# Performance work log

Measured on AMD Instinct MI355X. Metric: run time of the kernel, lower is better.

The kernel has to match this reference:

```python
import jax, jax.numpy as jnp
import numpy as np

B, S, D, H, DFF = 2, 2048, 1024, 16, 4096
DK = D // H
EPS = 1e-6
MASK_FILL = -1.0  # original code uses -1**9 == -1 (precedence bug), NOT -1e9


def layernorm(x, gamma, beta):
    # original: (x - mean) / (std + eps), std unbiased (torch default ddof=1), scalar gamma/beta
    mean = jnp.mean(x, axis=-1, keepdims=True)
    std = jnp.std(x, axis=-1, keepdims=True, ddof=1)
    return gamma * (x - mean) / (std + EPS) + beta


def setup_inputs() -> dict:
    key = jax.random.key(0)
    ks = jax.random.split(key, 12)
    sc = 0.02
    return {
        "x": jax.random.normal(ks[0], (B, S, D), jnp.float32),
        "src_mask": jnp.ones((B, 1, 1, S), jnp.int32),
        "wq": jax.random.normal(ks[1], (D, D), jnp.float32) * sc,
        "bq": jnp.zeros((D,), jnp.float32),
        "wk": jax.random.normal(ks[2], (D, D), jnp.float32) * sc,
        "bk": jnp.zeros((D,), jnp.float32),
        "wv": jax.random.normal(ks[3], (D, D), jnp.float32) * sc,
        "bv": jnp.zeros((D,), jnp.float32),
        "wo": jax.random.normal(ks[4], (D, D), jnp.float32) * sc,
        "bo": jnp.zeros((D,), jnp.float32),
        "w1": jax.random.normal(ks[5], (D, DFF), jnp.float32) * sc,
        "b1": jnp.zeros((DFF,), jnp.float32),
        "w2": jax.random.normal(ks[6], (DFF, D), jnp.float32) * sc,
        "b2": jnp.zeros((D,), jnp.float32),
        "g1": jnp.ones((), jnp.float32),
        "be1": jnp.zeros((), jnp.float32),
        "g2": jnp.ones((), jnp.float32),
        "be2": jnp.zeros((), jnp.float32),
    }


def reference(x, src_mask, wq, bq, wk, bk, wv, bv, wo, bo,
              w1, b1, w2, b2, g1, be1, g2, be2):
    # --- residual 1: pre-LN self-attention ---
    xn = layernorm(x, g1, be1)
    q = (xn @ wq + bq).reshape(B, S, H, DK).transpose(0, 2, 1, 3)  # [B,H,S,DK]
    k = (xn @ wk + bk).reshape(B, S, H, DK).transpose(0, 2, 1, 3)
    v = (xn @ wv + bv).reshape(B, S, H, DK).transpose(0, 2, 1, 3)
    scores = jnp.einsum('bhqd,bhkd->bhqk', q, k) / jnp.sqrt(jnp.float32(DK))
    scores = jnp.where(src_mask == 0, MASK_FILL, scores)
    attn = jax.nn.softmax(scores, axis=-1)
    ctx = jnp.einsum('bhqk,bhkd->bhqd', attn, v)
    ctx = ctx.transpose(0, 2, 1, 3).reshape(B, S, D)
    attn_out = ctx @ wo + bo
    x = x + attn_out  # dropout is identity in eval

    # --- residual 2: pre-LN feed-forward ---
    xn = layernorm(x, g2, be2)
    h = jax.nn.relu(xn @ w1 + b1)
    ff_out = h @ w2 + b2
    return x + ff_out
```

## Files before the change

### kernel.cpp

```cpp
#include <hip/hip_runtime.h>

typedef unsigned short u16;
typedef __bf16 bf16x8 __attribute__((ext_vector_type(8)));
typedef float f32x4 __attribute__((ext_vector_type(4)));
typedef float f32x16 __attribute__((ext_vector_type(16)));

#define AS1U(p) ((__attribute__((address_space(1))) unsigned int*)(p))
#define AS3U(p) ((__attribute__((address_space(3))) unsigned int*)(p))

__device__ __forceinline__ u16 f2bf(float f) {
  union { float f; unsigned int i; } c; c.f = f;
  return (u16)((c.i + 0x7FFFu + ((c.i >> 16) & 1u)) >> 16);
}
__device__ __forceinline__ u16 f2bf_trunc(float f) {
  union { float f; unsigned int i; } c; c.f = f;
  return (u16)(c.i >> 16);
}
__device__ __forceinline__ unsigned cvt_pk_bf16(float lo, float hi) {
  unsigned r;
  asm("v_cvt_pk_bf16_f32 %0, %1, %2" : "=v"(r) : "v"(lo), "v"(hi));
  return r;
}
__device__ __forceinline__ void plswap(unsigned& a, unsigned& b) {
  asm("v_permlane32_swap_b32 %0, %1" : "+v"(a), "+v"(b));
}

template <int BM, int BN, int BK, int OMODE>
__global__ __launch_bounds__(256) void gemm_bt(
    const u16* __restrict__ A, long lda,
    const u16* __restrict__ B, long ldb,
    void* __restrict__ Cv, long ldc,
    int K, float scale, const float* __restrict__ bias,
    const float* __restrict__ res, long ldres, int relu) {
  constexpr int WN = (BN == 128) ? 64 : 32;
  constexpr int MI = 4, NJ = WN / 16;
  constexpr int KK = BK / 32;
  __shared__ u16 As0[BM * BK], As1[BM * BK];
  __shared__ u16 Bs0[BN * BK], Bs1[BN * BK];
  const int t = threadIdx.x;
  const int w = t >> 6, l = t & 63;
  const int wr = w >> 1, wc = w & 1;
  const int quad = l >> 4, mlo = l & 15;
  const long row0 = (long)blockIdx.x * BM;
  const long col0 = (long)blockIdx.y * BN;

  f32x4 acc[MI][NJ] = {};

  auto stage = [&](u16 (&Ad)[BM * BK], u16 (&Bd)[BN * BK], int k0) {
    if (BK == 32) {
#pragma unroll
      for (int i = 0; i < BM / 64; i++) {
        int s = t + i * 256, r = s >> 2, c = s & 3;
        const u16* g = A + (row0 + r) * lda + k0 + c * 8;
        __builtin_amdgcn_global_load_lds(AS1U(g), AS3U(&Ad[s * 8]), 16, 0, 0);
      }
#pragma unroll
      for (int i = 0; i < BN / 64; i++) {
        int s = t + i * 256, r = s >> 2, c = s & 3;
        const u16* g = B + (col0 + r) * ldb + k0 + c * 8;
        __builtin_amdgcn_global_load_lds(AS1U(g), AS3U(&Bd[s * 8]), 16, 0, 0);
      }
    } else {
#pragma unroll
      for (int i = 0; i < BM / 32; i++) {
        int s = t + i * 256, r = s >> 3, c = s & 7;
        const u16* g = A + (row0 + r) * lda + k0 + (c ^ (r & 7)) * 8;
        __builtin_amdgcn_global_load_lds(AS1U(g), AS3U(&Ad[s * 8]), 16, 0, 0);
      }
#pragma unroll
      for (int i = 0; i < BN / 32; i++) {
        int s = t + i * 256, r = s >> 3, c = s & 7;
        const u16* g = B + (col0 + r) * ldb + k0 + (c ^ (r & 7)) * 8;
        __builtin_amdgcn_global_load_lds(AS1U(g), AS3U(&Bd[s * 8]), 16, 0, 0);
      }
    }
  };
  auto compute = [&](const u16 (&Asr)[BM * BK], const u16 (&Bsr)[BN * BK]) {
#pragma unroll
    for (int kk = 0; kk < KK; kk++) {
      bf16x8 a[MI], b[NJ];
#pragma unroll
      for (int i = 0; i < MI; i++) {
        int r = wr * 64 + i * 16 + mlo;
        a[i] = (BK == 32) ? *(const bf16x8*)&Asr[(r * 4 + quad) * 8]
                          : *(const bf16x8*)&Asr[(r * 8 + ((kk * 4 + quad) ^ (r & 7))) * 8];
      }
#pragma unroll
      for (int j = 0; j < NJ; j++) {
        int r = wc * WN + j * 16 + mlo;
        b[j] = (BK == 32) ? *(const bf16x8*)&Bsr[(r * 4 + quad) * 8]
                          : *(const bf16x8*)&Bsr[(r * 8 + ((kk * 4 + quad) ^ (r & 7))) * 8];
      }
#pragma unroll
      for (int i = 0; i < MI; i++)
#pragma unroll
        for (int j = 0; j < NJ; j++)
          acc[i][j] = __builtin_amdgcn_mfma_f32_16x16x32_bf16(a[i], b[j], acc[i][j], 0, 0, 0);
    }
  };

  stage(As0, Bs0, 0);
  for (int k0 = 0; k0 < K; k0 += 2 * BK) {
    __syncthreads();
    stage(As1, Bs1, k0 + BK);
    compute(As0, Bs0);
    __syncthreads();
    if (k0 + 2 * BK < K) stage(As0, Bs0, k0 + 2 * BK);
    compute(As1, Bs1);
  }

#pragma unroll
  for (int i = 0; i < MI; i++) {
#pragma unroll
    for (int j = 0; j < NJ; j++) {
      const long gn = col0 + wc * WN + j * 16 + mlo;
      const float bv = bias ? bias[gn] : 0.0f;
#pragma unroll
      for (int r = 0; r < 4; r++) {
        const long gm = row0 + wr * 64 + i * 16 + quad * 4 + r;
        float v = acc[i][j][r] * scale + bv;
        if (relu && v < 0.0f) v = 0.0f;
        if (res) v += res[gm * ldres + gn];
        if (OMODE == 0) ((float*)Cv)[gm * ldc + gn] = v;
        else ((u16*)Cv)[gm * ldc + gn] = f2bf(v);
      }
    }
  }
}

__global__ __launch_bounds__(256, 2) void flash_attn(
    const u16* __restrict__ QKV, const u16* __restrict__ VT,
    const int* __restrict__ mask, u16* __restrict__ ctx) {
  __shared__ u16 Ks[2][64 * 64];
  __shared__ u16 Vs[2][64 * 64];
  const int t = threadIdx.x;
  const int w = t >> 6, l = t & 63;
  const int hi = l >> 5, lq = l & 31, rx = lq & 7;
  const int z = blockIdx.z, b = z >> 4, h = z & 15;
  const long q0 = (long)blockIdx.x * 128;
  const u16* Qg = QKV + (long)b * (2048L * 3072) + h * 64;
  const u16* Kg = Qg + 1024;
  const u16* Vg = VT + (long)b * (1024L * 2048) + (long)(h * 64) * 2048;
  const int* mrow = mask + b * 2048;

#pragma unroll
  for (int i = 0; i < 2; i++) {
    int s = t + i * 256, r = s >> 3, c = s & 7;
    __builtin_amdgcn_global_load_lds(AS1U(Kg + (long)r * 3072 + (c ^ (r & 7)) * 8),
                                     AS3U(&Ks[0][s * 8]), 16, 0, 0);
    __builtin_amdgcn_global_load_lds(AS1U(Vg + (long)r * 2048 + (c ^ (r & 7)) * 8),
                                     AS3U(&Vs[0][s * 8]), 16, 0, 0);
  }

  const float CS = 0.125f * 1.44269504f;
  const float CM = -1.44269504f;

  bf16x8 aq[4];
#pragma unroll
  for (int kk = 0; kk < 4; kk++) {
    const u16* g = Qg + (q0 + w * 32 + lq) * 3072 + kk * 16 + hi * 8;
    union { uint4 u; bf16x8 v; u16 s[8]; } cc; cc.u = *(const uint4*)g;
#pragma unroll
    for (int e = 0; e < 8; e++) {
      union { unsigned u; float f; } qf; qf.u = (unsigned)cc.s[e] << 16;
      cc.s[e] = f2bf(qf.f * CS);
    }
    aq[kk] = cc.v;
  }

  unsigned am = 0;
  for (int it = 0; it < 32; ++it) {
    unsigned long long bmv = __ballot(mrow[it * 64 + l] != 0);
    am |= ((bmv == ~0ull) ? 1u : 0u) << it;
  }

  f32x16 o[2] = {}, den = {};
  union { u16 s[8]; bf16x8 v; } ones;
#pragma unroll
  for (int e = 0; e < 8; e++) ones.s[e] = 0x3F80;

  for (int it = 0; it < 32; ++it) {
    const int cur = it & 1;
    __syncthreads();
    if (it + 1 < 32) {
      const int nb = 1 - cur;
      const u16* Kg2 = Kg + (long)(it + 1) * 64 * 3072;
      const u16* Vg2 = Vg + (it + 1) * 64;
#pragma unroll
      for (int i2 = 0; i2 < 2; i2++) {
        int s = t + i2 * 256, r = s >> 3, c = s & 7;
        __builtin_amdgcn_global_load_lds(AS1U(Kg2 + (long)r * 3072 + (c ^ (r & 7)) * 8),
                                         AS3U(&Ks[nb][s * 8]), 16, 0, 0);
        __builtin_amdgcn_global_load_lds(AS1U(Vg2 + (long)r * 2048 + (c ^ (r & 7)) * 8),
                                         AS3U(&Vs[nb][s * 8]), 16, 0, 0);
      }
    }
    const bool allone = (am >> it) & 1u;
    unsigned long long bm = ~0ull;
    if (!allone) bm = __ballot(mrow[it * 64 + l] != 0);

    f32x16 sa[2];
    __builtin_amdgcn_s_setprio(1);
#pragma unroll
    for (int kt = 0; kt < 2; kt++) {
      f32x16 s0 = {};
      const int rk = kt * 32 + lq;
#pragma unroll
      for (int kk = 0; kk < 4; kk++) {
        bf16x8 ak = *(const bf16x8*)&Ks[cur][(rk * 8 + ((2 * kk + hi) ^ rx)) * 8];
        s0 = __builtin_amdgcn_mfma_f32_32x32x16_bf16(ak, aq[kk], s0, 0, 0, 0);
      }
      sa[kt] = s0;
    }
    __builtin_amdgcn_s_setprio(0);

#pragma unroll
    for (int kt = 0; kt < 2; kt++) {
      float p[16];
      if (allone) {
#pragma unroll
        for (int g = 0; g < 16; g++) p[g] = __builtin_amdgcn_exp2f(sa[kt][g]);
      } else {
#pragma unroll
        for (int g = 0; g < 16; g++) {
          const int k = kt * 32 + (g & 3) + 8 * (g >> 2) + 4 * hi;
          const float s = ((bm >> k) & 1) ? sa[kt][g] : CM;
          p[g] = __builtin_amdgcn_exp2f(s);
        }
      }
      unsigned wd[4][2];
#pragma unroll
      for (int g = 0; g < 4; g++) {
        wd[g][0] = cvt_pk_bf16(p[4 * g + 0], p[4 * g + 1]);
        wd[g][1] = cvt_pk_bf16(p[4 * g + 2], p[4 * g + 3]);
      }
#pragma unroll
      for (int c = 0; c < 2; c++) {
        plswap(wd[2 * c][0], wd[2 * c + 1][0]);
        plswap(wd[2 * c][1], wd[2 * c + 1][1]);
        union { unsigned u[4]; bf16x8 v; } pa;
        pa.u[0] = wd[2 * c][0];
        pa.u[1] = wd[2 * c][1];
        pa.u[2] = wd[2 * c + 1][0];
        pa.u[3] = wd[2 * c + 1][1];
        const int cg = kt * 2 + c;
        __builtin_amdgcn_s_setprio(1);
#pragma unroll
        for (int dt = 0; dt < 2; dt++) {
          const int rv = dt * 32 + lq;
          bf16x8 bv = *(const bf16x8*)&Vs[cur][(rv * 8 + ((2 * cg + hi) ^ rx)) * 8];
          o[dt] = __builtin_amdgcn_mfma_f32_32x32x16_bf16(pa.v, bv, o[dt], 0, 0, 0);
        }
        den = __builtin_amdgcn_mfma_f32_32x32x16_bf16(pa.v, ones.v, den, 0, 0, 0);
        __builtin_amdgcn_s_setprio(0);
      }
    }
  }

  u16* cb = ctx + (long)b * (2048L * 1024) + (q0 + w * 32) * 1024 + h * 64;
#pragma unroll
  for (int g = 0; g < 16; g++) {
    const int row = (g & 3) + 8 * (g >> 2) + 4 * hi;
    const float inv = 1.0f / den[g];
    cb[(long)row * 1024 + lq] = f2bf(o[0][g] * inv);
    cb[(long)row * 1024 + 32 + lq] = f2bf(o[1][g] * inv);
  }
}

__device__ __forceinline__ void ln_row(const float* __restrict__ x, u16* __restrict__ y,
                                       const float* __restrict__ g, const float* __restrict__ b,
                                       long row, float* ss, float* s2) {
  const float* xr = x + row * 1024;
  float v[4];
  float s = 0.f, sq = 0.f;
#pragma unroll
  for (int i = 0; i < 4; i++) {
    float f = xr[threadIdx.x + i * 256];
    v[i] = f; s += f; sq += f * f;
  }
#pragma unroll
  for (int o = 32; o > 0; o >>= 1) { s += __shfl_xor(s, o, 64); sq += __shfl_xor(sq, o, 64); }
  const int w = threadIdx.x >> 6;
  if ((threadIdx.x & 63) == 0) { ss[w] = s; s2[w] = sq; }
  __syncthreads();
  s = ss[0] + ss[1] + ss[2] + ss[3];
  sq = s2[0] + s2[1] + s2[2] + s2[3];
  const float mean = s * (1.0f / 1024.0f);
  float var = (sq - s * mean) * (1.0f / 1023.0f);
  var = fmaxf(var, 0.0f);
  const float sc = g[0] / (sqrtf(var) + 1e-6f);
  const float be = b[0];
#pragma unroll
  for (int i = 0; i < 4; i++)
    y[row * 1024 + threadIdx.x + i * 256] = f2bf((v[i] - mean) * sc + be);
}

__global__ __launch_bounds__(256) void ln_kernel(const float* __restrict__ x, u16* __restrict__ y,
                                                 const float* __restrict__ g, const float* __restrict__ b) {
  __shared__ float ss[4], s2[4];
  ln_row(x, y, g, b, blockIdx.x, ss, s2);
}

__global__ __launch_bounds__(256) void prep_kernel(
    const float* __restrict__ x, const float* __restrict__ g1, const float* __restrict__ be1,
    const float* __restrict__ wq, const float* __restrict__ wk, const float* __restrict__ wv,
    const float* __restrict__ wo, const float* __restrict__ w1, const float* __restrict__ w2,
    const float* __restrict__ bq, const float* __restrict__ bk, const float* __restrict__ bv,
    u16* __restrict__ xnH, u16* __restrict__ WqkvT, u16* __restrict__ woT,
    u16* __restrict__ w1T, u16* __restrict__ w2T, float* __restrict__ biasQKV) {
  __shared__ float tile[32][33];
  __shared__ float ss[4], s2[4];
  const int bid = blockIdx.x;
  if (bid >= 12300) {
    ln_row(x, xnH, g1, be1, bid - 12300, ss, s2);
    return;
  }
  if (bid >= 12288) {
    const int i = (bid - 12288) * 256 + threadIdx.x;
    if (i < 3072) biasQKV[i] = (i < 1024) ? bq[i] : ((i < 2048) ? bk[i - 1024] : bv[i - 2048]);
    return;
  }
  const float* in; u16* out; long ldin, ldo; int ti, tiles_x;
  if (bid < 1024)      { in = wq; out = WqkvT;                     ldin = 1024; ldo = 1024; ti = bid;        tiles_x = 32; }
  else if (bid < 2048) { in = wk; out = WqkvT + (size_t)1024*1024; ldin = 1024; ldo = 1024; ti = bid - 1024; tiles_x = 32; }
  else if (bid < 3072) { in = wv; out = WqkvT + (size_t)2048*1024; ldin = 1024; ldo = 1024; ti = bid - 2048; tiles_x = 32; }
  else if (bid < 4096) { in = wo; out = woT;                       ldin = 1024; ldo = 1024; ti = bid - 3072; tiles_x = 32; }
  else if (bid < 8192) { in = w1; out = w1T;                       ldin = 4096; ldo = 1024; ti = bid - 4096; tiles_x = 128; }
  else                 { in = w2; out = w2T;                       ldin = 1024; ldo = 4096; ti = bid - 8192; tiles_x = 32; }
  const int bx = (ti % tiles_x) * 32, by = (ti / tiles_x) * 32;
  const int tx = threadIdx.x & 31, ty = threadIdx.x >> 5;
#pragma unroll
  for (int i = 0; i < 32; i += 8) tile[ty + i][tx] = in[(long)(by + ty + i) * ldin + bx + tx];
  __syncthreads();
#pragma unroll
  for (int i = 0; i < 32; i += 8)
    out[(long)(bx + ty + i) * ldo + by + tx] = f2bf(tile[tx][ty + i]);
}

__global__ __launch_bounds__(256) void ttrans1(const u16* __restrict__ in, long ldin, long siz,
                                               u16* __restrict__ out, long ldo, long soz) {
  __shared__ u16 tile[32][33];
  const long zi = (long)blockIdx.z * siz, zo = (long)blockIdx.z * soz;
  const int bx = blockIdx.x * 32, by = blockIdx.y * 32;
  const int tx = threadIdx.x & 31, ty = threadIdx.x >> 5;
#pragma unroll
  for (int i = 0; i < 32; i += 8)
    tile[ty + i][tx] = in[zi + (long)(by + ty + i) * ldin + bx + tx];
  __syncthreads();
#pragma unroll
  for (int i = 0; i < 32; i += 8)
    out[zo + (long)(bx + ty + i) * ldo + by + tx] = tile[tx][ty + i];
}

extern "C" void kernel_launch(void* const* d_in, const int* in_sizes, int n_in,
                              void* d_out, int out_size, void* d_ws, size_t ws_size,
                              hipStream_t stream) {
  const float* x   = (const float*)d_in[0];
  const int*   msk = (const int*)d_in[1];
  const float* wq  = (const float*)d_in[2];
  const float* bq  = (const float*)d_in[3];
  const float* wk  = (const float*)d_in[4];
  const float* bk  = (const float*)d_in[5];
  const float* wv  = (const float*)d_in[6];
  const float* bv  = (const float*)d_in[7];
  const float* wo  = (const float*)d_in[8];
  const float* bo  = (const float*)d_in[9];
  const float* w1  = (const float*)d_in[10];
  const float* b1  = (const float*)d_in[11];
  const float* w2  = (const float*)d_in[12];
  const float* b2  = (const float*)d_in[13];
  const float* g1  = (const float*)d_in[14];
  const float* be1 = (const float*)d_in[15];
  const float* g2  = (const float*)d_in[16];
  const float* be2 = (const float*)d_in[17];
  float* out = (float*)d_out;

  char* basep = (char*)d_ws;
  size_t off = 0;
  auto au = [&](size_t nelem) -> u16* {
    u16* r = (u16*)(basep + off);
    off += ((nelem * 2) + 255) & ~(size_t)255;
    return r;
  };
  auto afp = [&](size_t nelem) -> float* {
    float* r = (float*)(basep + off);
    off += ((nelem * 4) + 255) & ~(size_t)255;
    return r;
  };

  u16* xnH  = au((size_t)4096 * 1024);
  u16* QKV  = au((size_t)4096 * 3072);
  u16* VTH  = au((size_t)2 * 1024 * 2048);
  u16* ctxH = au((size_t)4096 * 1024);
  float* x1 = afp((size_t)4096 * 1024);
  u16* hb   = au((size_t)4096 * 4096);
  u16* WqkvT = au((size_t)3072 * 1024);
  u16* woT  = au((size_t)1024 * 1024);
  u16* w1T  = au((size_t)4096 * 1024);
  u16* w2T  = au((size_t)1024 * 4096);
  float* biasQKV = afp(3072);

  const dim3 blk(256);

  prep_kernel<<<16396, blk, 0, stream>>>(x, g1, be1, wq, wk, wv, wo, w1, w2,
                                         bq, bk, bv, xnH, WqkvT, woT, w1T, w2T, biasQKV);

  gemm_bt<128, 128, 32, 2><<<dim3(32, 24), blk, 0, stream>>>(
      xnH, 1024, WqkvT, 1024, QKV, 3072, 1024, 1.0f,
      biasQKV, (const float*)0, 0, 0);

  ttrans1<<<dim3(32, 64, 2), blk, 0, stream>>>(
      QKV + 2048, 3072, (long)2048 * 3072, VTH, 2048, (long)1024 * 2048);

  flash_attn<<<dim3(16, 1, 32), blk, 0, stream>>>(QKV, VTH, msk, ctxH);

  gemm_bt<128, 64, 64, 0><<<dim3(32, 16), blk, 0, stream>>>(
      ctxH, 1024, woT, 1024, x1, 1024, 1024, 1.0f, bo, x, 1024, 0);

  ln_kernel<<<4096, blk, 0, stream>>>(x1, xnH, g2, be2);

  gemm_bt<128, 128, 32, 2><<<dim3(32, 32), blk, 0, stream>>>(
      xnH, 1024, w1T, 1024, hb, 4096, 1024, 1.0f,
      b1, (const float*)0, 0, 1);

  gemm_bt<128, 64, 64, 0><<<dim3(32, 16), blk, 0, stream>>>(
      hb, 4096, w2T, 4096, out, 1024, 4096, 1.0f, b2, x1, 1024, 0);
}
```

Measured before the change: 356.7 us.

## Add 256x128 triple-buffered direct-to-LDS MFMA GEMM for QKV and FF1

Introduces a new 512-thread GEMM kernel with 256x128 tiles and BK=64. It uses three LDS buffers filled by global_load_lds with an XOR swizzle, 32x32x16 bf16 MFMAs, and setprio around the math. It replaces the 128x128 GEMM for the QKV projection and the first FFN matmul, aiming for more data reuse per block and better overlap of loads with compute. The large LDS footprint limits residency to one block per CU, and the QKV grid leaves a partial wave.

```diff
diff --git a/kernel.cpp b/kernel.cpp
--- a/kernel.cpp
+++ b/kernel.cpp
@@ -23,6 +23,102 @@
 }
 __device__ __forceinline__ void plswap(unsigned& a, unsigned& b) {
   asm("v_permlane32_swap_b32 %0, %1" : "+v"(a), "+v"(b));
+}
+
+template <int OMODE>
+__global__ __launch_bounds__(512, 2) void gemm3(
+    const u16* __restrict__ A, long lda,
+    const u16* __restrict__ B, long ldb,
+    void* __restrict__ Cv, long ldc,
+    int K, const float* __restrict__ bias,
+    const float* __restrict__ res, long ldres, int relu) {
+  __shared__ u16 As[3][256 * 64];
+  __shared__ u16 Bs[3][128 * 64];
+  const int t = threadIdx.x;
+  const int w = t >> 6, l = t & 63;
+  const int hi = l >> 5, lq = l & 31;
+  const int wm = w >> 1, wn = w & 1;
+  const long row0 = (long)blockIdx.x * 256;
+  const long col0 = (long)blockIdx.y * 128;
+
+  auto stage = [&](int slot, int k0) {
+#pragma unroll
+    for (int i = 0; i < 4; i++) {
+      int s = t + i * 512, r = s >> 3, c = s & 7;
+      __builtin_amdgcn_global_load_lds(AS1U(A + (row0 + r) * lda + k0 + (c ^ (r & 7)) * 8),
+                                       AS3U(&As[slot][s * 8]), 16, 0, 0);
+    }
+#pragma unroll
+    for (int i = 0; i < 2; i++) {
+      int s = t + i * 512, r = s >> 3, c = s & 7;
+      __builtin_amdgcn_global_load_lds(AS1U(B + (col0 + r) * ldb + k0 + (c ^ (r & 7)) * 8),
+                                       AS3U(&Bs[slot][s * 8]), 16, 0, 0);
+    }
+  };
+
+  f32x16 acc[2][2] = {};
+  const int NT = K >> 6;
+
+  stage(0, 0);
+  stage(1, 64);
+  asm volatile("s_waitcnt vmcnt(6)" ::: "memory");
+  __builtin_amdgcn_s_barrier();
+  __builtin_amdgcn_sched_barrier(0);
+
+  int s0 = 0, s1 = 1, s2 = 2;
+  for (int kt = 0; kt < NT; kt++) {
+    if (kt + 2 < NT) stage(s2, (kt + 2) * 64);
+    bf16x8 a[2][4], b[2][4];
+#pragma unroll
+    for (int mi = 0; mi < 2; mi++) {
+      const int r = wm * 64 + mi * 32 + lq;
+#pragma unroll
+      for (int kk = 0; kk < 4; kk++)
+        a[mi][kk] = *(const bf16x8*)&As[s0][(r * 8 + ((kk * 2 + hi) ^ (r & 7))) * 8];
+    }
+#pragma unroll
+    for (int nj = 0; nj < 2; nj++) {
+      const int r = wn * 64 + nj * 32 + lq;
+#pragma unroll
+      for (int kk = 0; kk < 4; kk++)
+        b[nj][kk] = *(const bf16x8*)&Bs[s0][(r * 8 + ((kk * 2 + hi) ^ (r & 7))) * 8];
+    }
+    __builtin_amdgcn_s_setprio(1);
+#pragma unroll
+    for (int kk = 0; kk < 4; kk++)
+#pragma unroll
+      for (int mi = 0; mi < 2; mi++)
+#pragma unroll
+        for (int nj = 0; nj < 2; nj++)
+          acc[mi][nj] = __builtin_amdgcn_mfma_f32_32x32x16_bf16(a[mi][kk], b[nj][kk], acc[mi][nj], 0, 0, 0);
+    __builtin_amdgcn_s_setprio(0);
+    if (kt + 2 < NT) {
+      asm volatile("s_waitcnt vmcnt(6)" ::: "memory");
+    } else {
+      asm volatile("s_waitcnt vmcnt(0)" ::: "memory");
+    }
+    __builtin_amdgcn_s_barrier();
+    __builtin_amdgcn_sched_barrier(0);
+    const int tmp = s0; s0 = s1; s1 = s2; s2 = tmp;
+  }
+
+#pragma unroll
+  for (int nj = 0; nj < 2; nj++) {
+    const long gn = col0 + wn * 64 + nj * 32 + lq;
+    const float bv = bias ? bias[gn] : 0.0f;
+#pragma unroll
+    for (int mi = 0; mi < 2; mi++) {
+#pragma unroll
+      for (int g = 0; g < 16; g++) {
+        const long gm = row0 + wm * 64 + mi * 32 + (g & 3) + 8 * (g >> 2) + 4 * hi;
+        float v = acc[mi][nj][g] + bv;
+        if (relu && v < 0.0f) v = 0.0f;
+        if (res) v += res[gm * ldres + gn];
+        if (OMODE == 0) ((float*)Cv)[gm * ldc + gn] = v;
+        else ((u16*)Cv)[gm * ldc + gn] = f2bf(v);
+      }
+    }
+  }
 }
 
 template <int BM, int BN, int BK, int OMODE>
@@ -401,12 +497,13 @@
   float* biasQKV = afp(3072);
 
   const dim3 blk(256);
+  const dim3 blk5(512);
 
   prep_kernel<<<16396, blk, 0, stream>>>(x, g1, be1, wq, wk, wv, wo, w1, w2,
                                          bq, bk, bv, xnH, WqkvT, woT, w1T, w2T, biasQKV);
 
-  gemm_bt<128, 128, 32, 2><<<dim3(32, 24), blk, 0, stream>>>(
-      xnH, 1024, WqkvT, 1024, QKV, 3072, 1024, 1.0f,
+  gemm3<2><<<dim3(16, 24), blk5, 0, stream>>>(
+      xnH, 1024, WqkvT, 1024, QKV, 3072, 1024,
       biasQKV, (const float*)0, 0, 0);
 
   ttrans1<<<dim3(32, 64, 2), blk, 0, stream>>>(
@@ -419,8 +516,8 @@
 
   ln_kernel<<<4096, blk, 0, stream>>>(x1, xnH, g2, be2);
 
-  gemm_bt<128, 128, 32, 2><<<dim3(32, 32), blk, 0, stream>>>(
-      xnH, 1024, w1T, 1024, hb, 4096, 1024, 1.0f,
+  gemm3<2><<<dim3(16, 32), blk5, 0, stream>>>(
+      xnH, 1024, w1T, 1024, hb, 4096, 1024,
       b1, (const float*)0, 0, 1);
 
   gemm_bt<128, 64, 64, 0><<<dim3(32, 16), blk, 0, stream>>>(
```

Result: slower. 365.6 us (+2.5%).
